# Performance work log

Measured on AMD Instinct MI355X. Metric: run time of the kernel, lower is better.

Reference implementation:

```python
import jax, jax.numpy as jnp
import numpy as np

M_DIM = 1024
H_DIM = 1024
NEG = -1e9


def setup_inputs() -> dict:
    key = jax.random.key(0)
    ks = jax.random.split(key, 9)
    B, S = 4, 2048
    q = jax.random.normal(ks[0], (B, S, M_DIM), dtype=jnp.float32)
    k = jax.random.normal(ks[1], (B, S, M_DIM), dtype=jnp.float32)
    v = jax.random.normal(ks[2], (B, S, M_DIM), dtype=jnp.float32)
    attention_mask = jnp.ones((B, S), dtype=jnp.int32)
    sc = 1.0 / np.sqrt(M_DIM)
    Wq_w = jax.random.normal(ks[3], (H_DIM, M_DIM), dtype=jnp.float32) * sc
    Wq_b = jnp.zeros((H_DIM,), dtype=jnp.float32)
    Wk_w = jax.random.normal(ks[4], (H_DIM, M_DIM), dtype=jnp.float32) * sc
    Wk_b = jnp.zeros((H_DIM,), dtype=jnp.float32)
    Wv_w = jax.random.normal(ks[5], (H_DIM, M_DIM), dtype=jnp.float32) * sc
    Wv_b = jnp.zeros((H_DIM,), dtype=jnp.float32)
    return {"q": q, "k": k, "v": v, "attention_mask": attention_mask,
            "Wq_w": Wq_w, "Wq_b": Wq_b, "Wk_w": Wk_w, "Wk_b": Wk_b,
            "Wv_w": Wv_w, "Wv_b": Wv_b}


def reference(q, k, v, attention_mask, Wq_w, Wq_b, Wk_w, Wk_b, Wv_w, Wv_b):
    # Linear projections (torch Linear: x @ W.T + b)
    qh = jnp.einsum('bsm,hm->bsh', q, Wq_w) + Wq_b
    kh = jnp.einsum('bsm,hm->bsh', k, Wk_w) + Wk_b
    vh = jnp.einsum('bsm,hm->bsh', v, Wv_w) + Wv_b
    # Scaled dot-product scores: [B, Sq, Sk]
    scores = jnp.einsum('bqh,bkh->bqk', qh, kh) / jnp.sqrt(jnp.float32(H_DIM))
    # Padding mask: attention_mask [B, Sk] -> [B, 1, Sk]
    pad = attention_mask.astype(bool)[:, None, :]
    scores = jnp.where(pad, scores, NEG)
    # Causal mask (apply_mask=True)
    Sq, Sk = scores.shape[1], scores.shape[2]
    causal = jnp.tril(jnp.ones((Sq, Sk), dtype=bool))
    scores = jnp.where(causal[None, :, :], scores, NEG)
    attn = jax.nn.softmax(scores, axis=-1)
    out = jnp.einsum('bqk,bkh->bqh', attn, vh)
    # dropout is identity in eval mode
    return out
```

## Files before the change

kernel.cpp:

```cpp
#include <hip/hip_runtime.h>
#include <stdint.h>


typedef __attribute__((ext_vector_type(8))) short s8v;
typedef __attribute__((ext_vector_type(4))) float f4v;

__device__ __forceinline__ unsigned short f2bf(float f) {
    union { float f; unsigned u; } v; v.f = f;
    unsigned u = v.u;
    u = u + 0x7fffu + ((u >> 16) & 1u);
    return (unsigned short)(u >> 16);
}

__device__ __forceinline__ void gld_lds16(const void* gptr, void* lptr) {
    __builtin_amdgcn_global_load_lds(
        (const __attribute__((address_space(1))) unsigned int*)(uintptr_t)gptr,
        (__attribute__((address_space(3))) unsigned int*)(unsigned int)(uintptr_t)lptr,
        16, 0, 0);
}

__global__ __launch_bounds__(256) void convert_all(
    const float* __restrict__ q, const float* __restrict__ k, const float* __restrict__ v,
    const float* __restrict__ wq, const float* __restrict__ wk, const float* __restrict__ wv,
    unsigned short* __restrict__ qb, unsigned short* __restrict__ kb, unsigned short* __restrict__ vb,
    unsigned short* __restrict__ wqb, unsigned short* __restrict__ wkb, unsigned short* __restrict__ wvb)
{
    int b = blockIdx.x;
    const float* src; unsigned short* dst; int blk;
    if (b < 8192)       { src = q;  dst = qb;  blk = b; }
    else if (b < 16384) { src = k;  dst = kb;  blk = b - 8192; }
    else if (b < 24576) { src = v;  dst = vb;  blk = b - 16384; }
    else if (b < 25600) { src = wq; dst = wqb; blk = b - 24576; }
    else if (b < 26624) { src = wk; dst = wkb; blk = b - 25600; }
    else                { src = wv; dst = wvb; blk = b - 26624; }
    size_t idx = (size_t)blk * 1024 + (size_t)threadIdx.x * 4;
    float4 f = *(const float4*)(src + idx);
    ushort4 o = make_ushort4(f2bf(f.x), f2bf(f.y), f2bf(f.z), f2bf(f.w));
    *(ushort4*)(dst + idx) = o;
}

__global__ __launch_bounds__(256) void zero_f32(float* __restrict__ p, int n) {
    int i = blockIdx.x * 256 + threadIdx.x;
    if (i < n) p[i] = 0.f;
}

__device__ __forceinline__ void gemm_tiles(
    const unsigned short* __restrict__ A, int lda,
    const unsigned short* __restrict__ Bt, int ldb,
    int m0, int n0, int kTiles,
    unsigned short* As, unsigned short* Bs,
    f4v acc[4][4])
{
    const int t    = threadIdx.x;
    const int lane = t & 63;
    const int wave = t >> 6;
    const int wm   = (wave >> 1) * 64;
    const int wn   = (wave & 1) * 64;
    const int l15  = lane & 15;
    const int quad = lane >> 4;

    const int c0 = t, c1 = t + 256;
    unsigned short* As0 = As + (c0 & ~63) * 8;
    unsigned short* As1 = As + (c1 & ~63) * 8;
    unsigned short* Bs0 = Bs + (c0 & ~63) * 8;
    unsigned short* Bs1 = Bs + (c1 & ~63) * 8;
    const unsigned short* Ag0 = A  + (size_t)(m0 + (c0 >> 2)) * lda + (c0 & 3) * 8;
    const unsigned short* Ag1 = A  + (size_t)(m0 + (c1 >> 2)) * lda + (c1 & 3) * 8;
    const unsigned short* Bg0 = Bt + (size_t)(n0 + (c0 >> 2)) * ldb + (c0 & 3) * 8;
    const unsigned short* Bg1 = Bt + (size_t)(n0 + (c1 >> 2)) * ldb + (c1 & 3) * 8;

    const unsigned short* a_base = As + quad * 8;
    const unsigned short* b_base = Bs + quad * 8;

    for (int kt = 0; kt < kTiles; ++kt) {
        gld_lds16(Ag0, As0);
        gld_lds16(Ag1, As1);
        gld_lds16(Bg0, Bs0);
        gld_lds16(Bg1, Bs1);
        Ag0 += 32; Ag1 += 32; Bg0 += 32; Bg1 += 32;
        __syncthreads();
        s8v af[4], bf[4];
        #pragma unroll
        for (int i = 0; i < 4; ++i)
            af[i] = *(const s8v*)(a_base + (wm + i * 16 + l15) * 32);
        #pragma unroll
        for (int j = 0; j < 4; ++j)
            bf[j] = *(const s8v*)(b_base + (wn + j * 16 + l15) * 32);
        #pragma unroll
        for (int i = 0; i < 4; ++i)
            #pragma unroll
            for (int j = 0; j < 4; ++j)
                acc[i][j] = __builtin_amdgcn_mfma_f32_16x16x32_bf16(af[i], bf[j], acc[i][j], 0, 0, 0);
        __syncthreads();
    }
}

#define ACC_INIT  f4v acc[4][4]; { f4v z = {0.f,0.f,0.f,0.f}; \
    _Pragma("unroll") for (int i = 0; i < 4; ++i) \
    _Pragma("unroll") for (int j = 0; j < 4; ++j) acc[i][j] = z; }

#define LANE_VARS \
    const int lane = threadIdx.x & 63; const int wave = threadIdx.x >> 6; \
    const int wm = (wave >> 1) * 64;  const int wn = (wave & 1) * 64; \
    const int l15 = lane & 15;        const int quad = lane >> 4;

__global__ __launch_bounds__(256) void proj_kernel(
    const unsigned short* __restrict__ X, const unsigned short* __restrict__ W,
    const float* __restrict__ bias, unsigned short* __restrict__ Y, int transpose_out)
{
    __shared__ __align__(16) unsigned short As[128 * 32];
    __shared__ __align__(16) unsigned short Bs[128 * 32];
    const int m0 = blockIdx.y * 128;
    const int n0 = blockIdx.x * 128;
    ACC_INIT;
    gemm_tiles(X, 1024, W, 1024, m0, n0, 32, As, Bs, acc);
    LANE_VARS;
    #pragma unroll
    for (int i = 0; i < 4; ++i) {
        int row = m0 + wm + i * 16 + quad * 4;
        #pragma unroll
        for (int j = 0; j < 4; ++j) {
            int col = n0 + wn + j * 16 + l15;
            float bv = bias[col];
            if (!transpose_out) {
                #pragma unroll
                for (int r = 0; r < 4; ++r)
                    Y[(size_t)(row + r) * 1024 + col] = f2bf(acc[i][j][r] + bv);
            } else {
                int bb = row >> 11;
                int s  = row & 2047;
                ushort4 o = make_ushort4(f2bf(acc[i][j][0] + bv), f2bf(acc[i][j][1] + bv),
                                         f2bf(acc[i][j][2] + bv), f2bf(acc[i][j][3] + bv));
                *(ushort4*)(Y + (size_t)bb * (1024 * 2048) + (size_t)col * 2048 + s) = o;
            }
        }
    }
}

__global__ __launch_bounds__(256) void score_kernel(
    const unsigned short* __restrict__ QH, const unsigned short* __restrict__ KH,
    const int* __restrict__ mask, unsigned short* __restrict__ P, float* __restrict__ lsum)
{
    const int kt = blockIdx.x, qt = blockIdx.y, b = blockIdx.z;
    if (kt > qt) return;
    __shared__ __align__(16) unsigned short As[128 * 32];
    __shared__ __align__(16) unsigned short Bs[128 * 32];
    const unsigned short* A  = QH + (size_t)b * 2048 * 1024;
    const unsigned short* Bt = KH + (size_t)b * 2048 * 1024;
    unsigned short* Pb = P + (size_t)b * 2048 * 2048;
    float* lb = lsum + b * 2048;
    const int* mb = mask + b * 2048;
    const int m0 = qt * 128, n0 = kt * 128;
    ACC_INIT;
    gemm_tiles(A, 1024, Bt, 1024, m0, n0, 32, As, Bs, acc);
    LANE_VARS;
    float rs[4][4];
    #pragma unroll
    for (int i = 0; i < 4; ++i)
        #pragma unroll
        for (int r = 0; r < 4; ++r) rs[i][r] = 0.f;
    #pragma unroll
    for (int i = 0; i < 4; ++i) {
        int qbase = m0 + wm + i * 16 + quad * 4;
        #pragma unroll
        for (int j = 0; j < 4; ++j) {
            int kg = n0 + wn + j * 16 + l15;
            int mv = mb[kg];
            #pragma unroll
            for (int r = 0; r < 4; ++r) {
                float s = acc[i][j][r] * 0.03125f;
                float p = (mv && (kg <= qbase + r)) ? __expf(s) : 0.f;
                Pb[(size_t)(qbase + r) * 2048 + kg] = f2bf(p);
                rs[i][r] += p;
            }
        }
    }
    #pragma unroll
    for (int i = 0; i < 4; ++i)
        #pragma unroll
        for (int r = 0; r < 4; ++r) {
            float v_ = rs[i][r];
            v_ += __shfl_xor(v_, 1);
            v_ += __shfl_xor(v_, 2);
            v_ += __shfl_xor(v_, 4);
            v_ += __shfl_xor(v_, 8);
            if (l15 == 0)
                atomicAdd(&lb[m0 + wm + i * 16 + quad * 4 + r], v_);
        }
}

__global__ __launch_bounds__(256) void pv_kernel(
    const unsigned short* __restrict__ P, const unsigned short* __restrict__ VHT,
    const float* __restrict__ lsum, float* __restrict__ Out)
{
    const int nt = blockIdx.x, qt = blockIdx.y, b = blockIdx.z;
    __shared__ __align__(16) unsigned short As[128 * 32];
    __shared__ __align__(16) unsigned short Bs[128 * 32];
    const unsigned short* A  = P   + (size_t)b * 2048 * 2048;
    const unsigned short* Bt = VHT + (size_t)b * 1024 * 2048;
    const float* lb = lsum + b * 2048;
    float* Ob = Out + (size_t)b * 2048 * 1024;
    const int m0 = qt * 128, n0 = nt * 128;
    ACC_INIT;
    gemm_tiles(A, 2048, Bt, 2048, m0, n0, qt * 4 + 4, As, Bs, acc);
    LANE_VARS;
    #pragma unroll
    for (int i = 0; i < 4; ++i) {
        int q0 = m0 + wm + i * 16 + quad * 4;
        float inv[4];
        #pragma unroll
        for (int r = 0; r < 4; ++r) inv[r] = 1.0f / lb[q0 + r];
        #pragma unroll
        for (int j = 0; j < 4; ++j) {
            int h = n0 + wn + j * 16 + l15;
            #pragma unroll
            for (int r = 0; r < 4; ++r)
                Ob[(size_t)(q0 + r) * 1024 + h] = acc[i][j][r] * inv[r];
        }
    }
}

extern "C" void kernel_launch(void* const* d_in, const int* in_sizes, int n_in,
                              void* d_out, int out_size, void* d_ws, size_t ws_size,
                              hipStream_t stream)
{
    const float* q    = (const float*)d_in[0];
    const float* k    = (const float*)d_in[1];
    const float* v    = (const float*)d_in[2];
    const int*   mask = (const int*)d_in[3];
    const float* Wq   = (const float*)d_in[4];
    const float* bq   = (const float*)d_in[5];
    const float* Wk   = (const float*)d_in[6];
    const float* bk   = (const float*)d_in[7];
    const float* Wv   = (const float*)d_in[8];
    const float* bv   = (const float*)d_in[9];
    float* out = (float*)d_out;

    char* ws = (char*)d_ws;
    size_t off = 0;
    auto take = [&](size_t bytes) { char* p = ws + off; off += (bytes + 255) & ~(size_t)255; return p; };
    unsigned short* qb  = (unsigned short*)take(8192ull * 1024 * 2);
    unsigned short* kb  = (unsigned short*)take(8192ull * 1024 * 2);
    unsigned short* vb  = (unsigned short*)take(8192ull * 1024 * 2);
    unsigned short* wqb = (unsigned short*)take(1024ull * 1024 * 2);
    unsigned short* wkb = (unsigned short*)take(1024ull * 1024 * 2);
    unsigned short* wvb = (unsigned short*)take(1024ull * 1024 * 2);
    unsigned short* QH  = (unsigned short*)take(8192ull * 1024 * 2);
    unsigned short* KH  = (unsigned short*)take(8192ull * 1024 * 2);
    unsigned short* VHT = (unsigned short*)take(8192ull * 1024 * 2);
    unsigned short* P   = (unsigned short*)take(4ull * 2048 * 2048 * 2);
    float*          l   = (float*)take(4ull * 2048 * 4);

    zero_f32<<<32, 256, 0, stream>>>(l, 4 * 2048);
    convert_all<<<27648, 256, 0, stream>>>(q, k, v, Wq, Wk, Wv, qb, kb, vb, wqb, wkb, wvb);
    proj_kernel<<<dim3(8, 64), 256, 0, stream>>>(qb, wqb, bq, QH, 0);
    proj_kernel<<<dim3(8, 64), 256, 0, stream>>>(kb, wkb, bk, KH, 0);
    proj_kernel<<<dim3(8, 64), 256, 0, stream>>>(vb, wvb, bv, VHT, 1);
    score_kernel<<<dim3(16, 16, 4), 256, 0, stream>>>(QH, KH, mask, P, l);
    pv_kernel<<<dim3(8, 16, 4), 256, 0, stream>>>(P, VHT, l, out);
}
```

Baseline: 356.0 us.

## Split-K the causal PV GEMM with atomics and batch the three projections

The PV kernel now splits the K dimension of the longer causal rows into up to four chunks so work per block is more even. The partial results are accumulated into the output with float atomicAdd, and the output buffer is zeroed first in a combined zero kernel. Blocks are ordered heaviest-first, which is meant to reduce tail imbalance. The three projection GEMMs are merged into one launch using blockIdx.z, which fills more of the GPU and removes launch gaps. In exchange there is extra atomic traffic, a full output memset, and the summation order becomes nondeterministic.

After: 380.5 us. +6.9%, slower.

```diff
diff --git a/kernel.cpp b/kernel.cpp
--- a/kernel.cpp
+++ b/kernel.cpp
@@ -17,6 +17,14 @@
         (const __attribute__((address_space(1))) unsigned int*)(uintptr_t)gptr,
         (__attribute__((address_space(3))) unsigned int*)(unsigned int)(uintptr_t)lptr,
         16, 0, 0);
+}
+
+__global__ __launch_bounds__(256) void zero_ws(float4* __restrict__ out4, int n4,
+                                               float* __restrict__ l, int nl) {
+    int i = blockIdx.x * 256 + threadIdx.x;
+    if (i < n4) { out4[i] = make_float4(0.f, 0.f, 0.f, 0.f); return; }
+    int li = i - n4;
+    if (li < nl) l[li] = 0.f;
 }
 
 __global__ __launch_bounds__(256) void convert_all(
@@ -39,11 +47,6 @@
     *(ushort4*)(dst + idx) = o;
 }
 
-__global__ __launch_bounds__(256) void zero_f32(float* __restrict__ p, int n) {
-    int i = blockIdx.x * 256 + threadIdx.x;
-    if (i < n) p[i] = 0.f;
-}
-
 __device__ __forceinline__ void gemm_tiles(
     const unsigned short* __restrict__ A, int lda,
     const unsigned short* __restrict__ Bt, int ldb,
@@ -105,9 +108,19 @@
     const int l15 = lane & 15;        const int quad = lane >> 4;
 
 __global__ __launch_bounds__(256) void proj_kernel(
-    const unsigned short* __restrict__ X, const unsigned short* __restrict__ W,
-    const float* __restrict__ bias, unsigned short* __restrict__ Y, int transpose_out)
-{
+    const unsigned short* __restrict__ qb, const unsigned short* __restrict__ wqb,
+    const float* __restrict__ bq, unsigned short* __restrict__ QH,
+    const unsigned short* __restrict__ kb, const unsigned short* __restrict__ wkb,
+    const float* __restrict__ bk, unsigned short* __restrict__ KH,
+    const unsigned short* __restrict__ vb, const unsigned short* __restrict__ wvb,
+    const float* __restrict__ bv, unsigned short* __restrict__ VHT)
+{
+    const int z = blockIdx.z;
+    const unsigned short* X; const unsigned short* W; const float* bias; unsigned short* Y;
+    if (z == 0)      { X = qb; W = wqb; bias = bq; Y = QH; }
+    else if (z == 1) { X = kb; W = wkb; bias = bk; Y = KH; }
+    else             { X = vb; W = wvb; bias = bv; Y = VHT; }
+
     __shared__ __align__(16) unsigned short As[128 * 32];
     __shared__ __align__(16) unsigned short Bs[128 * 32];
     const int m0 = blockIdx.y * 128;
@@ -121,16 +134,16 @@
         #pragma unroll
         for (int j = 0; j < 4; ++j) {
             int col = n0 + wn + j * 16 + l15;
-            float bv = bias[col];
-            if (!transpose_out) {
+            float bvv = bias[col];
+            if (z != 2) {
                 #pragma unroll
                 for (int r = 0; r < 4; ++r)
-                    Y[(size_t)(row + r) * 1024 + col] = f2bf(acc[i][j][r] + bv);
+                    Y[(size_t)(row + r) * 1024 + col] = f2bf(acc[i][j][r] + bvv);
             } else {
                 int bb = row >> 11;
                 int s  = row & 2047;
-                ushort4 o = make_ushort4(f2bf(acc[i][j][0] + bv), f2bf(acc[i][j][1] + bv),
-                                         f2bf(acc[i][j][2] + bv), f2bf(acc[i][j][3] + bv));
+                ushort4 o = make_ushort4(f2bf(acc[i][j][0] + bvv), f2bf(acc[i][j][1] + bvv),
+                                         f2bf(acc[i][j][2] + bvv), f2bf(acc[i][j][3] + bvv));
                 *(ushort4*)(Y + (size_t)bb * (1024 * 2048) + (size_t)col * 2048 + s) = o;
             }
         }
@@ -193,16 +206,27 @@
     const unsigned short* __restrict__ P, const unsigned short* __restrict__ VHT,
     const float* __restrict__ lsum, float* __restrict__ Out)
 {
-    const int nt = blockIdx.x, qt = blockIdx.y, b = blockIdx.z;
+    const int nt = blockIdx.x, b = blockIdx.z;
+    const int y  = 39 - blockIdx.y;
+    int qt, s, S;
+    if      (y < 4)  { qt = y;                 s = 0;            S = 1; }
+    else if (y < 12) { qt = 4  + (y - 4) / 2;  s = (y - 4) % 2;  S = 2; }
+    else if (y < 24) { qt = 8  + (y - 12) / 3; s = (y - 12) % 3; S = 3; }
+    else             { qt = 12 + (y - 24) / 4; s = (y - 24) % 4; S = 4; }
+    const int kT     = 4 * qt + 4;
+    const int per    = (kT + S - 1) / S;
+    const int kstart = s * per;
+    const int kcount = min(per, kT - kstart);
+
     __shared__ __align__(16) unsigned short As[128 * 32];
     __shared__ __align__(16) unsigned short Bs[128 * 32];
-    const unsigned short* A  = P   + (size_t)b * 2048 * 2048;
-    const unsigned short* Bt = VHT + (size_t)b * 1024 * 2048;
+    const unsigned short* A  = P   + (size_t)b * 2048 * 2048 + (size_t)kstart * 32;
+    const unsigned short* Bt = VHT + (size_t)b * 1024 * 2048 + (size_t)kstart * 32;
     const float* lb = lsum + b * 2048;
     float* Ob = Out + (size_t)b * 2048 * 1024;
     const int m0 = qt * 128, n0 = nt * 128;
     ACC_INIT;
-    gemm_tiles(A, 2048, Bt, 2048, m0, n0, qt * 4 + 4, As, Bs, acc);
+    gemm_tiles(A, 2048, Bt, 2048, m0, n0, kcount, As, Bs, acc);
     LANE_VARS;
     #pragma unroll
     for (int i = 0; i < 4; ++i) {
@@ -215,7 +239,7 @@
             int h = n0 + wn + j * 16 + l15;
             #pragma unroll
             for (int r = 0; r < 4; ++r)
-                Ob[(size_t)(q0 + r) * 1024 + h] = acc[i][j][r] * inv[r];
+                atomicAdd(&Ob[(size_t)(q0 + r) * 1024 + h], acc[i][j][r] * inv[r]);
         }
     }
 }
@@ -251,11 +275,12 @@
     unsigned short* P   = (unsigned short*)take(4ull * 2048 * 2048 * 2);
     float*          l   = (float*)take(4ull * 2048 * 4);
 
-    zero_f32<<<32, 256, 0, stream>>>(l, 4 * 2048);
+    const int n4 = 8192 * 1024 / 4;
+    zero_ws<<<(n4 + 8192 + 255) / 256, 256, 0, stream>>>((float4*)out, n4, l, 4 * 2048);
     convert_all<<<27648, 256, 0, stream>>>(q, k, v, Wq, Wk, Wv, qb, kb, vb, wqb, wkb, wvb);
-    proj_kernel<<<dim3(8, 64), 256, 0, stream>>>(qb, wqb, bq, QH, 0);
-    proj_kernel<<<dim3(8, 64), 256, 0, stream>>>(kb, wkb, bk, KH, 0);
-    proj_kernel<<<dim3(8, 64), 256, 0, stream>>>(vb, wvb, bv, VHT, 1);
+    proj_kernel<<<dim3(8, 64, 3), 256, 0, stream>>>(qb, wqb, bq, QH,
+                                                    kb, wkb, bk, KH,
+                                                    vb, wvb, bv, VHT);
     score_kernel<<<dim3(16, 16, 4), 256, 0, stream>>>(QH, KH, mask, P, l);
-    pv_kernel<<<dim3(8, 16, 4), 256, 0, stream>>>(P, VHT, l, out);
-}
+    pv_kernel<<<dim3(8, 40, 4), 256, 0, stream>>>(P, VHT, l, out);
+}
```
